# Kernel optimization log

Measured on AMD Instinct MI355X. Metric: run time of the kernel, lower is better.

Reference implementation:

```python
import jax, jax.numpy as jnp
import numpy as np

N = 200000
C = 384
G = 383            # number of unique target ids (0..G-1 all present w.h.p.)
M = G + 1          # object_num = len(unique) + 1; must equal C for the original broadcast
EPS = 1e-5


def setup_inputs() -> dict:
    key = jax.random.key(0)
    k1, k2 = jax.random.split(key)
    pred_id = jax.random.normal(k1, (N, C), dtype=jnp.float32)
    target_id = jax.random.randint(k2, (N,), 0, G)
    return {"pred_id": pred_id, "target_id": target_id}


def reference(pred_id, target_id):
    seg = target_id  # ids are 0..G-1 and all present -> sorted unique == arange(G)
    dt = pred_id.dtype
    ones = jnp.ones((N,), dtype=dt)
    n_rows = jax.ops.segment_sum(ones, seg, num_segments=G)                 # [G] group sizes
    row_sum = jax.ops.segment_sum(pred_id.sum(axis=1), seg, num_segments=G)  # [G]
    cnt = n_rows * C                                                        # elements per group
    mean = row_sum / cnt                                                    # scalar mean per group
    centered = pred_id - mean[seg][:, None]
    ss = jax.ops.segment_sum((centered * centered).sum(axis=1), seg, num_segments=G)
    # torch .std() is unbiased over all n_i*C elements; 0 if group has a single row
    std = jnp.where(n_rows > 1, jnp.sqrt(ss / jnp.maximum(cnt - 1.0, 1.0)), 0.0)

    # pad the extra (always-zero) object slot -> object_proto/object_std have M rows
    proto = jnp.concatenate([mean, jnp.zeros((1,), dt)])   # [M]; each row of object_proto is constant
    stdv = jnp.concatenate([std, jnp.zeros((1,), dt)])     # [M]

    diff = proto[None, :] - proto[:, None]                 # [M,M] V_dist[x,a,:] is constant over C
    norm = jnp.abs(diff) * jnp.sqrt(jnp.asarray(C, dt))    # ||V_dist||_2 over C channels
    d = jax.lax.stop_gradient(diff / (norm + EPS))         # detached unit direction, [M,M]

    # object_std_i[x,a,b] = |std[a] * d[x,a]|; object_std_j[x,a,b] = |std[b] * d[x,a]|
    si = jnp.abs(stdv[None, :, None] * d[:, :, None])      # [M,M,M]
    sj = jnp.abs(stdv[None, None, :] * d[:, :, None])      # [M,M,M]
    s = si + sj
    V = s / (norm[None, :, :] + s + EPS)                   # V_dist_norm broadcast as [1,M,M]
    mask = jnp.triu(jnp.ones((M, M), dtype=bool), k=1)     # triu(diagonal=1) on last two dims
    V = jnp.where(mask[None, :, :], V, jnp.zeros((), dt))
    return V.mean()
```

## Files before the change

kernel.cpp:

```cpp
#include <hip/hip_runtime.h>
#include <math.h>

#define NROWS 200000
#define C 384
#define G 383
#define M 384
#define EPS 1e-5f
#define SQRTC 19.595917942265423f

#define NBLK1 1024
#define THR1 512
#define NWAVES ((NBLK1 * THR1) / 64)
#define NBLK2 24
#define NBLK4 576

#define WS_PART  0
#define WS_S2    (WS_PART + NBLK1 * 1152)
#define WS_PROTO (WS_S2 + 8 * 1152)
#define WS_STD   (WS_PROTO + 384)
#define WS_P3    (WS_STD + 384)
#define WS_CTR   (WS_P3 + NBLK4)

__global__ __launch_bounds__(THR1) void stats_kernel(const float4* __restrict__ pred4,
                                                     const int* __restrict__ tgt,
                                                     float* __restrict__ ws,
                                                     int n_rows) {
    __shared__ float lc[384], ls[384], lq[384];
    const int tid = threadIdx.x;
    if (blockIdx.x == 0 && tid == 0) {
        unsigned int* ctr = (unsigned int*)(ws + WS_CTR);
        ctr[0] = 0u;
        ctr[1] = 0u;
    }
    for (int i = tid; i < 384; i += THR1) { lc[i] = 0.f; ls[i] = 0.f; lq[i] = 0.f; }
    __syncthreads();

    const int lane = tid & 63;
    const int wv   = (blockIdx.x * THR1 + tid) >> 6;

    for (int row = wv; row < n_rows; row += NWAVES) {
        const float4* rp = pred4 + (size_t)row * 96;
        const int seg = tgt[row];
        float4 v0 = rp[lane];
        float s = (v0.x + v0.y) + (v0.z + v0.w);
        float q = fmaf(v0.x, v0.x, fmaf(v0.y, v0.y, fmaf(v0.z, v0.z, v0.w * v0.w)));
        if (lane < 32) {
            float4 v1 = rp[64 + lane];
            s += (v1.x + v1.y) + (v1.z + v1.w);
            q += fmaf(v1.x, v1.x, fmaf(v1.y, v1.y, fmaf(v1.z, v1.z, v1.w * v1.w)));
        }
#pragma unroll
        for (int off = 32; off > 0; off >>= 1) {
            s += __shfl_down(s, off);
            q += __shfl_down(q, off);
        }
        if (lane == 0) {
            atomicAdd(&lc[seg], 1.0f);
            atomicAdd(&ls[seg], s);
            atomicAdd(&lq[seg], q);
        }
    }
    __syncthreads();

    float* dst = ws + (size_t)blockIdx.x * 1152;
    for (int i = tid; i < 384; i += THR1) {
        dst[i]       = lc[i];
        dst[384 + i] = ls[i];
        dst[768 + i] = lq[i];
    }
}

__global__ __launch_bounds__(384) void reduce_finalize_kernel(float* __restrict__ ws) {
    __shared__ int is_last;
    const int t   = blockIdx.x * 384 + threadIdx.x;
    const int j   = t % 1152;
    const int sub = t / 1152;
    float acc = 0.f;
#pragma unroll 8
    for (int b = sub; b < NBLK1; b += 8)
        acc += ws[WS_PART + (size_t)b * 1152 + j];
    ws[WS_S2 + sub * 1152 + j] = acc;

    __threadfence();
    __syncthreads();
    if (threadIdx.x == 0) {
        unsigned int* ctr = (unsigned int*)(ws + WS_CTR);
        is_last = (atomicAdd(&ctr[0], 1u) == NBLK2 - 1);
    }
    __syncthreads();
    if (!is_last) return;
    __threadfence();

    const int g = threadIdx.x;
    float cnt_r = 0.f, sum = 0.f, ss = 0.f;
#pragma unroll
    for (int sub2 = 0; sub2 < 8; ++sub2) {
        const float* s2 = ws + WS_S2 + sub2 * 1152;
        cnt_r += s2[g];
        sum   += s2[384 + g];
        ss    += s2[768 + g];
    }
    float mean = 0.f, sd = 0.f;
    if (g < G && cnt_r > 0.5f) {
        float cnt = cnt_r * (float)C;
        mean = sum / cnt;
        if (cnt_r > 1.5f) {
            float cs    = ss - cnt * mean * mean;
            float denom = fmaxf(cnt - 1.0f, 1.0f);
            sd = sqrtf(fmaxf(cs / denom, 0.f));
        }
    }
    ws[WS_PROTO + g] = mean;
    ws[WS_STD + g]   = sd;
}

__global__ __launch_bounds__(256) void triple_write_kernel(float* __restrict__ ws,
                                                           float* __restrict__ out) {
    __shared__ float sp[M];
    __shared__ float sst[M];
    __shared__ float wsum[4];
    __shared__ int is_last;
    const int tid = threadIdx.x;

    for (int i = tid; i < M; i += 256) {
        sp[i]  = ws[WS_PROTO + i];
        sst[i] = ws[WS_STD + i];
    }
    __syncthreads();

    const int idx = blockIdx.x * 256 + tid;
    const int a   = idx / M;
    const int x   = idx - a * M;
    float partial = 0.f;
    {
        const float pa = sp[a];
        const float sa = sst[a];
        const float u  = fabsf(pa - sp[x]);
        const float tt = u / (u * SQRTC + EPS);
        const float tsa = tt * sa;
#pragma unroll 4
        for (int b = a + 1; b < M; ++b) {
            float nab = fabsf(sp[b] - pa) * SQRTC;
            float s   = fmaf(tt, sst[b], tsa);
            partial += s * __builtin_amdgcn_rcpf(nab + s + EPS);
        }
    }

#pragma unroll
    for (int off = 32; off > 0; off >>= 1)
        partial += __shfl_down(partial, off);
    if ((tid & 63) == 0) wsum[tid >> 6] = partial;
    __syncthreads();
    if (tid == 0) {
        ws[WS_P3 + blockIdx.x] = wsum[0] + wsum[1] + wsum[2] + wsum[3];
        __threadfence();
        unsigned int* ctr = (unsigned int*)(ws + WS_CTR);
        is_last = (atomicAdd(&ctr[1], 1u) == NBLK4 - 1);
    }
    __syncthreads();
    if (!is_last) return;
    __threadfence();

    float v = ws[WS_P3 + tid] + ws[WS_P3 + 256 + tid];
    if (tid < 64) v += ws[WS_P3 + 512 + tid];
#pragma unroll
    for (int off = 32; off > 0; off >>= 1)
        v += __shfl_down(v, off);
    __shared__ float fsum[4];
    if ((tid & 63) == 0) fsum[tid >> 6] = v;
    __syncthreads();
    if (tid == 0) {
        float acc = (fsum[0] + fsum[1]) + (fsum[2] + fsum[3]);
        out[0] = acc / ((float)M * (float)M * (float)M);
    }
}

extern "C" void kernel_launch(void* const* d_in, const int* in_sizes, int n_in,
                              void* d_out, int out_size, void* d_ws, size_t ws_size,
                              hipStream_t stream) {
    const float4* pred4 = (const float4*)d_in[0];
    const int*    tgt   = (const int*)d_in[1];
    float* ws  = (float*)d_ws;
    float* out = (float*)d_out;
    const int n_rows = in_sizes[1];

    stats_kernel<<<NBLK1, THR1, 0, stream>>>(pred4, tgt, ws, n_rows);
    reduce_finalize_kernel<<<NBLK2, 384, 0, stream>>>(ws);
    triple_write_kernel<<<NBLK4, 256, 0, stream>>>(ws, out);
}
```

Before: 431.1 us.

## Fuse partial-stat reduction into triple-sum kernel with spin-wait flag

```diff
diff --git a/kernel.cpp b/kernel.cpp
--- a/kernel.cpp
+++ b/kernel.cpp
@@ -11,7 +11,7 @@
 #define NBLK1 1024
 #define THR1 512
 #define NWAVES ((NBLK1 * THR1) / 64)
-#define NBLK2 24
+#define NBLKR 36
 #define NBLK4 576
 
 #define WS_PART  0
@@ -27,10 +27,9 @@
                                                      int n_rows) {
     __shared__ float lc[384], ls[384], lq[384];
     const int tid = threadIdx.x;
-    if (blockIdx.x == 0 && tid == 0) {
+    if (blockIdx.x == 0 && tid < 3) {
         unsigned int* ctr = (unsigned int*)(ws + WS_CTR);
-        ctr[0] = 0u;
-        ctr[1] = 0u;
+        ctr[tid] = 0u;
     }
     for (int i = tid; i < 384; i += THR1) { lc[i] = 0.f; ls[i] = 0.f; lq[i] = 0.f; }
     __syncthreads();
@@ -70,57 +69,72 @@
     }
 }
 
-__global__ __launch_bounds__(384) void reduce_finalize_kernel(float* __restrict__ ws) {
-    __shared__ int is_last;
-    const int t   = blockIdx.x * 384 + threadIdx.x;
-    const int j   = t % 1152;
-    const int sub = t / 1152;
-    float acc = 0.f;
-#pragma unroll 8
-    for (int b = sub; b < NBLK1; b += 8)
-        acc += ws[WS_PART + (size_t)b * 1152 + j];
-    ws[WS_S2 + sub * 1152 + j] = acc;
-
-    __threadfence();
-    __syncthreads();
-    if (threadIdx.x == 0) {
-        unsigned int* ctr = (unsigned int*)(ws + WS_CTR);
-        is_last = (atomicAdd(&ctr[0], 1u) == NBLK2 - 1);
-    }
-    __syncthreads();
-    if (!is_last) return;
-    __threadfence();
-
-    const int g = threadIdx.x;
-    float cnt_r = 0.f, sum = 0.f, ss = 0.f;
-#pragma unroll
-    for (int sub2 = 0; sub2 < 8; ++sub2) {
-        const float* s2 = ws + WS_S2 + sub2 * 1152;
-        cnt_r += s2[g];
-        sum   += s2[384 + g];
-        ss    += s2[768 + g];
-    }
-    float mean = 0.f, sd = 0.f;
-    if (g < G && cnt_r > 0.5f) {
-        float cnt = cnt_r * (float)C;
-        mean = sum / cnt;
-        if (cnt_r > 1.5f) {
-            float cs    = ss - cnt * mean * mean;
-            float denom = fmaxf(cnt - 1.0f, 1.0f);
-            sd = sqrtf(fmaxf(cs / denom, 0.f));
-        }
-    }
-    ws[WS_PROTO + g] = mean;
-    ws[WS_STD + g]   = sd;
-}
-
-__global__ __launch_bounds__(256) void triple_write_kernel(float* __restrict__ ws,
-                                                           float* __restrict__ out) {
+__global__ __launch_bounds__(256) void tail_kernel(float* __restrict__ ws,
+                                                   float* __restrict__ out) {
     __shared__ float sp[M];
     __shared__ float sst[M];
     __shared__ float wsum[4];
     __shared__ int is_last;
+    unsigned int* ctr = (unsigned int*)(ws + WS_CTR);
     const int tid = threadIdx.x;
+    const int blk = blockIdx.x;
+
+    if (blk < NBLKR) {
+        const int t   = blk * 256 + tid;
+        const int j   = t % 1152;
+        const int sub = t / 1152;
+        float acc = 0.f;
+#pragma unroll 8
+        for (int b = sub; b < NBLK1; b += 8)
+            acc += ws[WS_PART + (size_t)b * 1152 + j];
+        ws[WS_S2 + sub * 1152 + j] = acc;
+
+        __threadfence();
+        __syncthreads();
+        if (tid == 0)
+            is_last = (atomicAdd(&ctr[0], 1u) == NBLKR - 1);
+        __syncthreads();
+        if (is_last) {
+            __threadfence();
+            for (int g = tid; g < 384; g += 256) {
+                float cnt_r = 0.f, sum = 0.f, ss = 0.f;
+#pragma unroll
+                for (int sub2 = 0; sub2 < 8; ++sub2) {
+                    const float* s2 = ws + WS_S2 + sub2 * 1152;
+                    cnt_r += s2[g];
+                    sum   += s2[384 + g];
+                    ss    += s2[768 + g];
+                }
+                float mean = 0.f, sd = 0.f;
+                if (g < G && cnt_r > 0.5f) {
+                    float cnt = cnt_r * (float)C;
+                    mean = sum / cnt;
+                    if (cnt_r > 1.5f) {
+                        float cs    = ss - cnt * mean * mean;
+                        float denom = fmaxf(cnt - 1.0f, 1.0f);
+                        sd = sqrtf(fmaxf(cs / denom, 0.f));
+                    }
+                }
+                ws[WS_PROTO + g] = mean;
+                ws[WS_STD + g]   = sd;
+            }
+            __syncthreads();
+            if (tid == 0) {
+                __threadfence();
+                __hip_atomic_store(&ctr[2], 1u, __ATOMIC_RELEASE,
+                                   __HIP_MEMORY_SCOPE_AGENT);
+            }
+        }
+    }
+
+    if (tid == 0) {
+        while (__hip_atomic_load(&ctr[2], __ATOMIC_ACQUIRE,
+                                 __HIP_MEMORY_SCOPE_AGENT) == 0u) {
+            __builtin_amdgcn_s_sleep(8);
+        }
+        __threadfence();
+    }
+    __syncthreads();
 
     for (int i = tid; i < M; i += 256) {
         sp[i]  = ws[WS_PROTO + i];
@@ -128,7 +142,7 @@
     }
     __syncthreads();
 
-    const int idx = blockIdx.x * 256 + tid;
+    const int idx = blk * 256 + tid;
     const int a   = idx / M;
     const int x   = idx - a * M;
     float partial = 0.f;
@@ -152,9 +166,8 @@
     if ((tid & 63) == 0) wsum[tid >> 6] = partial;
     __syncthreads();
     if (tid == 0) {
-        ws[WS_P3 + blockIdx.x] = wsum[0] + wsum[1] + wsum[2] + wsum[3];
+        ws[WS_P3 + blk] = wsum[0] + wsum[1] + wsum[2] + wsum[3];
         __threadfence();
-        unsigned int* ctr = (unsigned int*)(ws + WS_CTR);
         is_last = (atomicAdd(&ctr[1], 1u) == NBLK4 - 1);
     }
     __syncthreads();
@@ -185,6 +198,5 @@
     const int n_rows = in_sizes[1];
 
     stats_kernel<<<NBLK1, THR1, 0, stream>>>(pred4, tgt, ws, n_rows);
-    reduce_finalize_kernel<<<NBLK2, 384, 0, stream>>>(ws);
-    triple_write_kernel<<<NBLK4, 256, 0, stream>>>(ws, out);
+    tail_kernel<<<NBLK4, 256, 0, stream>>>(ws, out);
 }
```

After: 554.9 us. +28.7%, slower.
